# Kernel tuning notes

Hardware: AMD Instinct MI355X
Metric: run time of the kernel (lower is better)

The kernel has to match this reference:

```python
import jax, jax.numpy as jnp
import numpy as np

D_MODEL = 1024
NUM_HEADS = 16

def _dense_params(key, d_in, d_out):
    kw, _ = jax.random.split(key)
    # flax default: lecun_normal kernel, zeros bias
    W = jax.random.normal(kw, (d_in, d_out), dtype=jnp.float32) / np.sqrt(d_in)
    b = jnp.zeros((d_out,), dtype=jnp.float32)
    return W, b

def setup_inputs() -> dict:
    key = jax.random.key(0)
    ks = jax.random.split(key, 8)
    B, Tx, Tc = 2, 2048, 2048
    x = jax.random.normal(ks[0], (B, Tx, D_MODEL), dtype=jnp.float32)
    context = jax.random.normal(ks[1], (B, Tc, D_MODEL), dtype=jnp.float32)
    Wq, bq = _dense_params(ks[2], D_MODEL, D_MODEL)
    Wks, bks = _dense_params(ks[3], D_MODEL, D_MODEL)
    Wvs, bvs = _dense_params(ks[4], D_MODEL, D_MODEL)
    Wkc, bkc = _dense_params(ks[5], D_MODEL, D_MODEL)
    Wvc, bvc = _dense_params(ks[6], D_MODEL, D_MODEL)
    Wo, bo = _dense_params(ks[7], D_MODEL, D_MODEL)
    return {"x": x, "context": context,
            "Wq": Wq, "bq": bq, "Wks": Wks, "bks": bks, "Wvs": Wvs, "bvs": bvs,
            "Wkc": Wkc, "bkc": bkc, "Wvc": Wvc, "bvc": bvc, "Wo": Wo, "bo": bo}

def _split_heads(t, H):
    B, T, C = t.shape
    return t.reshape(B, T, H, C // H).transpose(0, 2, 1, 3)  # [B,H,T,hd]

def reference(x, context, Wq, bq, Wks, bks, Wvs, bvs, Wkc, bkc, Wvc, bvc, Wo, bo):
    H = NUM_HEADS
    head_dim = D_MODEL // H
    q = x @ Wq + bq
    k = jnp.concatenate([x @ Wks + bks, context @ Wkc + bkc], axis=1)
    v = jnp.concatenate([x @ Wvs + bvs, context @ Wvc + bvc], axis=1)
    q = _split_heads(q, H)  # [B,H,Tq,hd]
    k = _split_heads(k, H)  # [B,H,Tk,hd]
    v = _split_heads(v, H)
    attn = jnp.einsum('bhqd,bhkd->bhqk', q, k) / jnp.sqrt(jnp.float32(head_dim))
    attn = jax.nn.softmax(attn, axis=-1)
    out = jnp.einsum('bhqk,bhkd->bhqd', attn, v)
    B, _, Tq, _ = out.shape
    out = out.transpose(0, 2, 1, 3).reshape(B, Tq, D_MODEL)
    return out @ Wo + bo
```

## Files before the change

### kernel.cpp

```cpp
#include <hip/hip_runtime.h>
#include <hip/hip_bf16.h>
#include <math.h>


typedef _Float16 f16;
typedef _Float16 f16x8 __attribute__((ext_vector_type(8)));
typedef _Float16 f16x4v __attribute__((ext_vector_type(4)));
typedef _Float16 f16x2 __attribute__((ext_vector_type(2)));
typedef float    f32x4 __attribute__((ext_vector_type(4)));
typedef float    f32x16 __attribute__((ext_vector_type(16)));
typedef unsigned u32x4v __attribute__((ext_vector_type(4)));

#define MFMA_F16(a, b, c)  __builtin_amdgcn_mfma_f32_16x16x32_f16((a), (b), (c), 0, 0, 0)
#define MFMA32_F16(a, b, c) __builtin_amdgcn_mfma_f32_32x32x16_f16((a), (b), (c), 0, 0, 0)

#define QSCALE 0.18033688011112042f

__device__ __forceinline__ void glds16(const f16* g, f16* l) {
    __builtin_amdgcn_global_load_lds(
        (const __attribute__((address_space(1))) void*)g,
        (__attribute__((address_space(3))) void*)l, 16, 0, 0);
}

__device__ __forceinline__ unsigned pk16(float a, float b) {
    f16x2 t = { (f16)a, (f16)b };
    return __builtin_bit_cast(unsigned, t);
}

__global__ __launch_bounds__(256) void prep(
    const float4* __restrict__ x, const float4* __restrict__ ctx,
    f16x4v* __restrict__ xb, f16x4v* __restrict__ cb,
    const float* __restrict__ W0, const float* __restrict__ W1,
    const float* __restrict__ W2, const float* __restrict__ W3,
    const float* __restrict__ W4, const float* __restrict__ W5,
    f16* __restrict__ wt)
{
    if (blockIdx.x < 8192) {
        const int n4 = (2 * 2048 * 1024) / 4;
        int i = blockIdx.x * 256 + threadIdx.x;
        float4 v;
        f16x4v* dst;
        if (i < n4) { v = x[i];        dst = xb + i; }
        else        { v = ctx[i - n4]; dst = cb + (i - n4); }
        f16x4v h = { (f16)v.x, (f16)v.y, (f16)v.z, (f16)v.w };
        *dst = h;
        return;
    }
    const int idx = blockIdx.x - 8192;
    const int z = idx >> 10, rem = idx & 1023;
    const float* Ws[6] = { W0, W1, W2, W3, W4, W5 };
    const float* W = Ws[z];
    f16* Wt = wt + (size_t)z * (1024 * 1024);

    __shared__ float tile[32][33];
    const int tx = threadIdx.x & 31, ty = threadIdx.x >> 5;
    const int n0 = (rem & 31) * 32, k0 = (rem >> 5) * 32;

#pragma unroll
    for (int i = 0; i < 4; ++i) {
        int r = i * 8 + ty;
        tile[r][tx] = W[(size_t)(k0 + r) * 1024 + n0 + tx];
    }
    __syncthreads();
#pragma unroll
    for (int i = 0; i < 4; ++i) {
        int r = i * 8 + ty;
        Wt[(size_t)(n0 + r) * 1024 + k0 + tx] = (f16)tile[tx][r];
    }
}

#define GEMM_PROLOGUE(BN)                                                     \
    const int m0 = blockIdx.x * 128, n0 = blockIdx.y * (BN);                  \
    const int tid = threadIdx.x;                                              \
    const int w = tid >> 6, lane = tid & 63, quad = lane >> 4, l15 = lane & 15;\
    const int wm = (w >> 1) * 64, wn = (w & 1) * ((BN) / 2);                  \
    const int qsw = (quad ^ ((l15 >> 1) & 3)) * 8;                            \
    int gA[2], gB[(BN) / 64];                                                 \
    _Pragma("unroll")                                                         \
    for (int p = 0; p < 2; ++p) {                                             \
        int s = tid + p * 256;                                                \
        int r = (s >> 2) & 127, c = (s & 3) ^ ((s >> 3) & 3);                 \
        gA[p] = (m0 + r) * 1024 + c * 8;                                      \
    }                                                                         \
    _Pragma("unroll")                                                         \
    for (int p = 0; p < (BN) / 64; ++p) {                                     \
        int s = tid + p * 256;                                                \
        int r = (s >> 2) & ((BN) - 1), c = (s & 3) ^ ((s >> 3) & 3);          \
        gB[p] = (n0 + r) * 1024 + c * 8;                                      \
    }

#define GEMM_STAGE_TO(BN, buf, koff)                                          \
    _Pragma("unroll")                                                         \
    for (int p = 0; p < 2; ++p)                                               \
        glds16(&A[gA[p] + (koff)], &As[buf][(p * 256 + w * 64) * 8]);         \
    _Pragma("unroll")                                                         \
    for (int p = 0; p < (BN) / 64; ++p)                                       \
        glds16(&Bt[gB[p] + (koff)], &Bs[buf][(p * 256 + w * 64) * 8]);

__global__ __launch_bounds__(256) void proj_gemm(
    const f16* __restrict__ xb, const f16* __restrict__ cb,
    const f16* __restrict__ wt,
    const float* __restrict__ bq, const float* __restrict__ bks,
    const float* __restrict__ bkc, const float* __restrict__ bvs,
    const float* __restrict__ bvc,
    f16* __restrict__ qbuf, f16* __restrict__ kbuf, f16* __restrict__ vbuf)
{
    __shared__ alignas(16) f16 As[2][128 * 32];
    __shared__ alignas(16) f16 Bs[2][128 * 32];

    const int z = blockIdx.z;
    const f16* A = (z == 0 || z == 1 || z == 3) ? xb : cb;
    const int wslot = (z == 0) ? 0 : (z == 1) ? 1 : (z == 2) ? 3 : (z == 3) ? 2 : 4;
    const f16* Bt = wt + (size_t)wslot * 1048576;
    const float* bias = (z == 0) ? bq : (z == 1) ? bks : (z == 2) ? bkc
                        : (z == 3) ? bvs : bvc;
    const int roff = (z == 2 || z == 4) ? 2048 : 0;

    GEMM_PROLOGUE(128)
    f32x4 acc[4][4] = {};

    GEMM_STAGE_TO(128, 0, 0)

    for (int k0 = 0; k0 < 1024; k0 += 32) {
        const int cur = (k0 >> 5) & 1;
        __syncthreads();
        if (k0 + 32 < 1024) {
            GEMM_STAGE_TO(128, cur ^ 1, k0 + 32)
        }
        f16x8 a[4], b[4];
#pragma unroll
        for (int i = 0; i < 4; ++i)
            a[i] = *(const f16x8*)&As[cur][(wm + i * 16 + l15) * 32 + qsw];
#pragma unroll
        for (int i = 0; i < 4; ++i)
            b[i] = *(const f16x8*)&Bs[cur][(wn + i * 16 + l15) * 32 + qsw];
#pragma unroll
        for (int mi = 0; mi < 4; ++mi)
#pragma unroll
            for (int ni = 0; ni < 4; ++ni)
                acc[mi][ni] = MFMA_F16(a[mi], b[ni], acc[mi][ni]);
    }

#pragma unroll
    for (int mi = 0; mi < 4; ++mi) {
#pragma unroll
        for (int r = 0; r < 4; ++r) {
            int row = m0 + wm + mi * 16 + quad * 4 + r;
            int b_ = row >> 11, tok = row & 2047;
#pragma unroll
            for (int ni = 0; ni < 4; ++ni) {
                int col = n0 + wn + ni * 16 + l15;
                float v = acc[mi][ni][r] + bias[col];
                int bh = b_ * 16 + (col >> 6);
                int tg = roff + tok;
                if (z == 0) {
                    qbuf[((size_t)bh * 2048 + tok) * 64 + (col & 63)] = (f16)(v * QSCALE);
                } else if (z <= 2) {
                    kbuf[(size_t)bh * 262144 + (size_t)(tg >> 6) * 4096
                         + (size_t)((col >> 5) & 1) * 2048 + (tg & 63) * 32 + (col & 31)] = (f16)v;
                } else {
                    vbuf[(size_t)bh * 262144 + (size_t)tg * 64 + (col & 63)] = (f16)v;
                }
            }
        }
    }
}

__global__ __launch_bounds__(256) void transpose_v(
    const f16* __restrict__ vbuf, f16* __restrict__ vt)
{
    const int t = threadIdx.x;
    const int mt = t >> 3, md = t & 7;
    const int tok0 = blockIdx.x * 256 + mt * 8;
    const int z = blockIdx.y;
    f16x8 in[8];
#pragma unroll
    for (int i = 0; i < 8; ++i)
        in[i] = *(const f16x8*)&vbuf[((size_t)z * 4096 + tok0 + i) * 64 + md * 8];
    f16x8 ov[8];
#pragma unroll
    for (int j = 0; j < 8; ++j)
#pragma unroll
        for (int i = 0; i < 8; ++i) ov[j][i] = in[i][j];
    const int kt = tok0 >> 6, kks = (tok0 >> 5) & 1, kko = tok0 & 31;
#pragma unroll
    for (int j = 0; j < 8; ++j)
        *(f16x8*)&vt[(size_t)z * 262144 + (size_t)kt * 4096 + kks * 2048
                     + (md * 8 + j) * 32 + kko] = ov[j];
}

__global__ __launch_bounds__(256, 4) void attn_kernel(
    const f16* __restrict__ q, const f16* __restrict__ kb,
    const f16* __restrict__ vtb, f16* __restrict__ o01,
    f16* __restrict__ o23, float* __restrict__ lsplit)
{
    __shared__ alignas(16) f16 K_lds[4096];
    __shared__ alignas(16) f16 V_lds[4096];

    const int tid = threadIdx.x;
    const int w = tid >> 6, lane = tid & 63;
    const int l31 = lane & 31, h = lane >> 5;
    const int bh = blockIdx.x, qt = blockIdx.y, sp = blockIdx.z;
    const int qbase = qt * 128;

    f16x8 qa[4];
    {
        const size_t qrow = ((size_t)bh * 2048 + qbase + w * 32 + l31) * 64;
#pragma unroll
        for (int kc = 0; kc < 4; ++kc)
            qa[kc] = *(const f16x8*)&q[qrow + kc * 16 + h * 8];
    }

    f32x16 o_acc[2] = {};
    float l_part = 0.f;

    const f16* ktile = kb + (size_t)bh * 262144 + (size_t)sp * 65536;
    const f16* vtile = vtb + (size_t)bh * 262144 + (size_t)sp * 65536;

    const int sco = ((tid >> 2) * 4 + ((tid & 3) ^ ((tid >> 3) & 3))) * 8;
    const int ksw = (l31 >> 1) & 3;
    const int wslot = w * 512;
    const int lslot = wslot + lane * 8;

    glds16(ktile + sco,        &K_lds[wslot]);
    glds16(ktile + 2048 + sco, &K_lds[2048 + wslot]);
    glds16(vtile + sco,        &V_lds[wslot]);
    glds16(vtile + 2048 + sco, &V_lds[2048 + wslot]);

    for (int kt = 0; kt < 16; ++kt) {
        __syncthreads();

        ktile += 4096; vtile += 4096;
        f16x8 kn0, kn1, vn0, vn1;
        if (kt != 15) {
            kn0 = *(const f16x8*)&ktile[sco];
            kn1 = *(const f16x8*)&ktile[2048 + sco];
            vn0 = *(const f16x8*)&vtile[sco];
            vn1 = *(const f16x8*)&vtile[2048 + sco];
        }

#pragma unroll
        for (int mt = 0; mt < 2; ++mt) {
            f32x16 s = {};
            __builtin_amdgcn_s_setprio(1);
#pragma unroll
            for (int kc = 0; kc < 4; ++kc) {
                f16x8 ka = *(const f16x8*)&K_lds[(kc >> 1) * 2048
                             + (mt * 32 + l31) * 32
                             + ((((kc & 1) * 2 + h) ^ ksw)) * 8];
                s = MFMA32_F16(ka, qa[kc], s);
            }
            __builtin_amdgcn_s_setprio(0);

            float pe[16];
#pragma unroll
            for (int i = 0; i < 16; ++i) pe[i] = __builtin_amdgcn_exp2f(s[i]);

            {
                float t0 = (pe[0] + pe[1]) + (pe[2] + pe[3]);
                float t1 = (pe[4] + pe[5]) + (pe[6] + pe[7]);
                float t2 = (pe[8] + pe[9]) + (pe[10] + pe[11]);
                float t3 = (pe[12] + pe[13]) + (pe[14] + pe[15]);
                l_part += (t0 + t1) + (t2 + t3);
            }

#pragma unroll
            for (int c = 0; c < 2; ++c) {
                const int cb = c * 8;
                unsigned X0 = pk16(pe[cb + 0], pe[cb + 1]);
                unsigned X1 = pk16(pe[cb + 2], pe[cb + 3]);
                unsigned Y0 = pk16(pe[cb + 4], pe[cb + 5]);
                unsigned Y1 = pk16(pe[cb + 6], pe[cb + 7]);
                auto r0 = __builtin_amdgcn_permlane32_swap(X0, Y0, false, false);
                auto r1 = __builtin_amdgcn_permlane32_swap(X1, Y1, false, false);
                u32x4v pw;
                pw[0] = r0[0]; pw[1] = r1[0]; pw[2] = r0[1]; pw[3] = r1[1];
                f16x8 pfrag = __builtin_bit_cast(f16x8, pw);

                const int kchunk = mt * 2 + c;
                __builtin_amdgcn_s_setprio(1);
#pragma unroll
                for (int db = 0; db < 2; ++db) {
                    f16x8 va = *(const f16x8*)&V_lds[(kchunk >> 1) * 2048
                                 + (db * 32 + l31) * 32
                                 + (((((kchunk & 1) * 2 + h)) ^ ksw)) * 8];
                    o_acc[db] = MFMA32_F16(va, pfrag, o_acc[db]);
                }
                __builtin_amdgcn_s_setprio(0);
            }
        }

        __syncthreads();
        if (kt != 15) {
            *(f16x8*)&K_lds[lslot]        = kn0;
            *(f16x8*)&K_lds[2048 + lslot] = kn1;
            *(f16x8*)&V_lds[lslot]        = vn0;
            *(f16x8*)&V_lds[2048 + lslot] = vn1;
        }
    }

    float lf = l_part + __shfl_xor(l_part, 32, 64);
    float inv = 1.0f / lf;
    const int row = w * 32 + l31;
    if (h == 0) lsplit[((size_t)sp * 32 + bh) * 2048 + qbase + row] = lf;
    f16* ob = (sp & 2) ? o23 : o01;
    const size_t obase =
        (((size_t)(sp & 1) * 32 + bh) * 2048 + qbase + row) * 64;
#pragma unroll
    for (int db = 0; db < 2; ++db) {
#pragma unroll
        for (int g = 0; g < 4; ++g) {
            f16x4v ov;
#pragma unroll
            for (int i = 0; i < 4; ++i)
                ov[i] = (f16)(o_acc[db][g * 4 + i] * inv);
            *(f16x4v*)&ob[obase + db * 32 + g * 8 + h * 4] = ov;
        }
    }
}

__global__ __launch_bounds__(256) void combine(
    const f16* __restrict__ o01, const f16* __restrict__ o23,
    const float* __restrict__ lsplit, f16* __restrict__ abuf)
{
    int idx = blockIdx.x * 256 + threadIdx.x;
    int d8 = idx & 7;
    int row = (idx >> 3) & 2047;
    int bh = idx >> 14;
    int b = bh >> 4, h = bh & 15;
    const size_t rb = ((size_t)bh * 2048 + row) * 64 + d8 * 8;
    const size_t spstride = (size_t)32 * 2048 * 64;
    const int lrow = bh * 2048 + row;
    float l0 = lsplit[lrow];
    float l1 = lsplit[65536 + lrow];
    float l2 = lsplit[131072 + lrow];
    float l3 = lsplit[196608 + lrow];
    float inv = 1.0f / (((l0 + l1) + (l2 + l3)));
    f16x8 a0 = *(const f16x8*)&o01[rb];
    f16x8 a1 = *(const f16x8*)&o01[spstride + rb];
    f16x8 a2 = *(const f16x8*)&o23[rb];
    f16x8 a3 = *(const f16x8*)&o23[spstride + rb];
    float w0 = l0 * inv, w1 = l1 * inv, w2 = l2 * inv, w3 = l3 * inv;
    f16x8 out;
#pragma unroll
    for (int j = 0; j < 8; ++j)
        out[j] = (f16)(w0 * (float)a0[j] + w1 * (float)a1[j]
                     + w2 * (float)a2[j] + w3 * (float)a3[j]);
    *(f16x8*)&abuf[((size_t)(b * 2048 + row)) * 1024 + h * 64 + d8 * 8] = out;
}

__global__ __launch_bounds__(256) void out_gemm(
    const f16* __restrict__ abuf, const f16* __restrict__ wt5,
    const float* __restrict__ bo, float* __restrict__ out)
{
    __shared__ alignas(16) f16 As[2][128 * 32];
    __shared__ alignas(16) f16 Bs[2][64 * 32];

    const f16* A = abuf;
    const f16* Bt = wt5;

    GEMM_PROLOGUE(64)
    f32x4 acc[4][2] = {};

    GEMM_STAGE_TO(64, 0, 0)

    for (int k0 = 0; k0 < 1024; k0 += 32) {
        const int cur = (k0 >> 5) & 1;
        __syncthreads();
        if (k0 + 32 < 1024) {
            GEMM_STAGE_TO(64, cur ^ 1, k0 + 32)
        }
        f16x8 a[4], b[2];
#pragma unroll
        for (int i = 0; i < 4; ++i)
            a[i] = *(const f16x8*)&As[cur][(wm + i * 16 + l15) * 32 + qsw];
#pragma unroll
        for (int i = 0; i < 2; ++i)
            b[i] = *(const f16x8*)&Bs[cur][(wn + i * 16 + l15) * 32 + qsw];
#pragma unroll
        for (int mi = 0; mi < 4; ++mi)
#pragma unroll
            for (int ni = 0; ni < 2; ++ni)
                acc[mi][ni] = MFMA_F16(a[mi], b[ni], acc[mi][ni]);
    }

#pragma unroll
    for (int mi = 0; mi < 4; ++mi) {
#pragma unroll
        for (int r = 0; r < 4; ++r) {
            int row = m0 + wm + mi * 16 + quad * 4 + r;
#pragma unroll
            for (int ni = 0; ni < 2; ++ni) {
                int col = n0 + wn + ni * 16 + l15;
                out[(size_t)row * 1024 + col] = acc[mi][ni][r] + bo[col];
            }
        }
    }
}

extern "C" void kernel_launch(void* const* d_in, const int* in_sizes, int n_in,
                              void* d_out, int out_size, void* d_ws, size_t ws_size,
                              hipStream_t stream)
{
    (void)in_sizes; (void)n_in; (void)out_size; (void)ws_size;

    const float* x    = (const float*)d_in[0];
    const float* ctx  = (const float*)d_in[1];
    const float* Wq   = (const float*)d_in[2];  const float* bq  = (const float*)d_in[3];
    const float* Wks  = (const float*)d_in[4];  const float* bks = (const float*)d_in[5];
    const float* Wvs  = (const float*)d_in[6];  const float* bvs = (const float*)d_in[7];
    const float* Wkc  = (const float*)d_in[8];  const float* bkc = (const float*)d_in[9];
    const float* Wvc  = (const float*)d_in[10]; const float* bvc = (const float*)d_in[11];
    const float* Wo   = (const float*)d_in[12]; const float* bo  = (const float*)d_in[13];

    char* ws = (char*)d_ws;
    f16*   xb     = (f16*)(ws + 0);
    f16*   cb     = (f16*)(ws + 8388608);
    f16*   vt     = (f16*)(ws + 0);
    f16*   wt     = (f16*)(ws + 16777216);
    float* lsplit = (float*)(ws + 16777216);
    f16*   qbuf   = (f16*)(ws + 29360128);
    f16*   kbuf   = (f16*)(ws + 37748736);
    f16*   vbuf   = (f16*)(ws + 54525952);
    f16*   o01    = (f16*)(ws + 54525952);
    f16*   abuf   = (f16*)(ws + 71303168);
    f16*   o23    = (f16*)d_out;

    prep<<<14336, 256, 0, stream>>>((const float4*)x, (const float4*)ctx,
                                    (f16x4v*)xb, (f16x4v*)cb,
                                    Wq, Wks, Wvs, Wkc, Wvc, Wo, wt);

    proj_gemm<<<dim3(32, 8, 5), 256, 0, stream>>>(
        xb, cb, wt, bq, bks, bkc, bvs, bvc, qbuf, kbuf, vbuf);

    transpose_v<<<dim3(16, 32), 256, 0, stream>>>(vbuf, vt);

    attn_kernel<<<dim3(32, 16, 4), 256, 0, stream>>>(qbuf, kbuf, vt, o01, o23, lsplit);

    combine<<<2048, 256, 0, stream>>>(o01, o23, lsplit, abuf);

    out_gemm<<<dim3(32, 16), 256, 0, stream>>>(abuf, wt + 5 * 1048576, bo, (float*)d_out);
}
```

Measured before the change: 309.2 us.

## Load K/V fragments directly from global memory and swizzle attention block order

```diff
diff --git a/kernel.cpp b/kernel.cpp
--- a/kernel.cpp
+++ b/kernel.cpp
@@ -194,13 +194,13 @@
     const f16* __restrict__ vtb, f16* __restrict__ o01,
     f16* __restrict__ o23, float* __restrict__ lsplit)
 {
-    __shared__ alignas(16) f16 K_lds[4096];
-    __shared__ alignas(16) f16 V_lds[4096];
-
     const int tid = threadIdx.x;
     const int w = tid >> 6, lane = tid & 63;
     const int l31 = lane & 31, h = lane >> 5;
-    const int bh = blockIdx.x, qt = blockIdx.y, sp = blockIdx.z;
+
+    const int lin = blockIdx.x;
+    const int swz = (lin & 7) * 256 + (lin >> 3);
+    const int qt = swz & 15, bh = (swz >> 4) & 31, sp = swz >> 9;
     const int qbase = qt * 128;
 
     f16x8 qa[4];
@@ -214,42 +214,32 @@
     f32x16 o_acc[2] = {};
     float l_part = 0.f;
 
-    const f16* ktile = kb + (size_t)bh * 262144 + (size_t)sp * 65536;
-    const f16* vtile = vtb + (size_t)bh * 262144 + (size_t)sp * 65536;
-
-    const int sco = ((tid >> 2) * 4 + ((tid & 3) ^ ((tid >> 3) & 3))) * 8;
-    const int ksw = (l31 >> 1) & 3;
-    const int wslot = w * 512;
-    const int lslot = wslot + lane * 8;
-
-    glds16(ktile + sco,        &K_lds[wslot]);
-    glds16(ktile + 2048 + sco, &K_lds[2048 + wslot]);
-    glds16(vtile + sco,        &V_lds[wslot]);
-    glds16(vtile + 2048 + sco, &V_lds[2048 + wslot]);
-
+    const f16* kp = kb  + (size_t)bh * 262144 + (size_t)sp * 65536 + l31 * 32 + h * 8;
+    const f16* vp = vtb + (size_t)bh * 262144 + (size_t)sp * 65536 + l31 * 32 + h * 8;
+
+#pragma unroll 2
     for (int kt = 0; kt < 16; ++kt) {
-        __syncthreads();
-
-        ktile += 4096; vtile += 4096;
-        f16x8 kn0, kn1, vn0, vn1;
-        if (kt != 15) {
-            kn0 = *(const f16x8*)&ktile[sco];
-            kn1 = *(const f16x8*)&ktile[2048 + sco];
-            vn0 = *(const f16x8*)&vtile[sco];
-            vn1 = *(const f16x8*)&vtile[2048 + sco];
-        }
-
 #pragma unroll
         for (int mt = 0; mt < 2; ++mt) {
+            f16x8 ka[4];
+#pragma unroll
+            for (int kc = 0; kc < 4; ++kc)
+                ka[kc] = *(const f16x8*)&kp[(kc >> 1) * 2048 + mt * 1024 + (kc & 1) * 16];
+            f16x8 va[2][2];
+#pragma unroll
+            for (int c = 0; c < 2; ++c)
+#pragma unroll
+                for (int db = 0; db < 2; ++db) {
+                    const int kchunk = mt * 2 + c;
+                    va[c][db] = *(const f16x8*)&vp[(kchunk >> 1) * 2048
+                                 + db * 1024 + (kchunk & 1) * 16];
+                }
+
             f32x16 s = {};
             __builtin_amdgcn_s_setprio(1);
 #pragma unroll
-            for (int kc = 0; kc < 4; ++kc) {
-                f16x8 ka = *(const f16x8*)&K_lds[(kc >> 1) * 2048
-                             + (mt * 32 + l31) * 32
-                             + ((((kc & 1) * 2 + h) ^ ksw)) * 8];
-                s = MFMA32_F16(ka, qa[kc], s);
-            }
+            for (int kc = 0; kc < 4; ++kc)
+                s = MFMA32_F16(ka[kc], qa[kc], s);
             __builtin_amdgcn_s_setprio(0);
 
             float pe[16];
@@ -277,26 +267,14 @@
                 pw[0] = r0[0]; pw[1] = r1[0]; pw[2] = r0[1]; pw[3] = r1[1];
                 f16x8 pfrag = __builtin_bit_cast(f16x8, pw);
 
-                const int kchunk = mt * 2 + c;
                 __builtin_amdgcn_s_setprio(1);
 #pragma unroll
-                for (int db = 0; db < 2; ++db) {
-                    f16x8 va = *(const f16x8*)&V_lds[(kchunk >> 1) * 2048
-                                 + (db * 32 + l31) * 32
-                                 + (((((kchunk & 1) * 2 + h)) ^ ksw)) * 8];
-                    o_acc[db] = MFMA32_F16(va, pfrag, o_acc[db]);
-                }
+                for (int db = 0; db < 2; ++db)
+                    o_acc[db] = MFMA32_F16(va[c][db], pfrag, o_acc[db]);
                 __builtin_amdgcn_s_setprio(0);
             }
         }
-
-        __syncthreads();
-        if (kt != 15) {
-            *(f16x8*)&K_lds[lslot]        = kn0;
-            *(f16x8*)&K_lds[2048 + lslot] = kn1;
-            *(f16x8*)&V_lds[lslot]        = vn0;
-            *(f16x8*)&V_lds[2048 + lslot] = vn1;
-        }
+        kp += 4096; vp += 4096;
     }
 
     float lf = l_part + __shfl_xor(l_part, 32, 64);
@@ -435,7 +413,7 @@
 
     transpose_v<<<dim3(16, 32), 256, 0, stream>>>(vbuf, vt);
 
-    attn_kernel<<<dim3(32, 16, 4), 256, 0, stream>>>(qbuf, kbuf, vt, o01, o23, lsplit);
+    attn_kernel<<<2048, 256, 0, stream>>>(qbuf, kbuf, vt, o01, o23, lsplit);
 
     combine<<<2048, 256, 0, stream>>>(o01, o23, lsplit, abuf);
 
```

After: 354.6 us. 14.7% more time.
